# Kernel tuning notes

Hardware: AMD Instinct MI355X
Metric: run time of the kernel (lower is better)

## Reference

```python
import jax, jax.numpy as jnp
import numpy as np

D_MODEL = 1024
N_HEADS = 16
D_K = D_MODEL // N_HEADS


def setup_inputs() -> dict:
    key = jax.random.key(0)
    ks = jax.random.split(key, 7)
    B, T = 4, 2048
    scale = 1.0 / np.sqrt(D_MODEL)
    x = jax.random.normal(ks[0], (B, T, D_MODEL), dtype=jnp.float32)
    Wq = jax.random.uniform(ks[1], (D_MODEL, D_MODEL), jnp.float32, -scale, scale)
    Wk = jax.random.uniform(ks[2], (D_MODEL, D_MODEL), jnp.float32, -scale, scale)
    Wv = jax.random.uniform(ks[3], (D_MODEL, D_MODEL), jnp.float32, -scale, scale)
    bq = jax.random.uniform(ks[4], (D_MODEL,), jnp.float32, -scale, scale)
    bk = jax.random.uniform(ks[5], (D_MODEL,), jnp.float32, -scale, scale)
    bv = jax.random.uniform(ks[6], (D_MODEL,), jnp.float32, -scale, scale)
    return {"x": x, "Wq": Wq, "bq": bq, "Wk": Wk, "bk": bk, "Wv": Wv, "bv": bv}


def reference(x, Wq, bq, Wk, bk, Wv, bv):
    B, T, _ = x.shape
    # QKV projections -> (B, H, T, d_k)
    def split_heads(y):
        return y.reshape(B, T, N_HEADS, D_K).transpose(0, 2, 1, 3)
    Q = split_heads(x @ Wq + bq)
    K = split_heads(x @ Wk + bk)
    V = split_heads(x @ Wv + bv)
    scores = jnp.einsum('bhqd,bhkd->bhqk', Q, K) / jnp.sqrt(jnp.float32(D_K))
    # additive causal mask: -inf above the diagonal
    causal = jnp.tril(jnp.ones((T, T), dtype=bool))
    scores = jnp.where(causal, scores, -jnp.inf)
    attn = jax.nn.softmax(scores, axis=-1)
    out = jnp.einsum('bhqk,bhkd->bhqd', attn, V)
    return out.transpose(0, 2, 1, 3).reshape(B, T, D_MODEL)
```

## Files before the change

### kernel.cpp

```cpp
#include <hip/hip_runtime.h>
#include <hip/hip_bf16.h>

#define DM 1024
#define NH 16
#define DK 64
#define TT 2048
#define NBATCH 4
#define BT 8192

typedef __attribute__((ext_vector_type(8))) short short8;
typedef __attribute__((ext_vector_type(4))) float f32x4;
typedef unsigned short u16;

#define MFMA(a,b,c) __builtin_amdgcn_mfma_f32_16x16x32_bf16((a),(b),(c),0,0,0)

#define QSCALE 0.18033688011112684f

#define EXP2(x) __builtin_amdgcn_exp2f(x)

__device__ __forceinline__ u16 f2bf(float f){
  union { float f; unsigned u; } v; v.f = f;
  return (u16)((v.u + 0x7fffu + ((v.u >> 16) & 1u)) >> 16);
}

__device__ __forceinline__ unsigned cvtpk(float lo, float hi){
  unsigned r;
  asm("v_cvt_pk_bf16_f32 %0, %1, %2" : "=v"(r) : "v"(lo), "v"(hi));
  return r;
}

__device__ __forceinline__ void gload16(const void* g, void* l){
  __builtin_amdgcn_global_load_lds((__attribute__((address_space(1))) void*)(g),
                                   (__attribute__((address_space(3))) void*)(l), 16, 0, 0);
}

__device__ __forceinline__ float plmax(float x){
#if __has_builtin(__builtin_amdgcn_permlane16_swap) && __has_builtin(__builtin_amdgcn_permlane32_swap)
  auto r = __builtin_amdgcn_permlane16_swap(__float_as_uint(x), __float_as_uint(x), false, false);
  x = fmaxf(__uint_as_float(r[0]), __uint_as_float(r[1]));
  auto r2 = __builtin_amdgcn_permlane32_swap(__float_as_uint(x), __float_as_uint(x), false, false);
  x = fmaxf(__uint_as_float(r2[0]), __uint_as_float(r2[1]));
#else
  x = fmaxf(x, __shfl_xor(x, 16, 64));
  x = fmaxf(x, __shfl_xor(x, 32, 64));
#endif
  return x;
}

__device__ __forceinline__ float plsum(float x){
#if __has_builtin(__builtin_amdgcn_permlane16_swap) && __has_builtin(__builtin_amdgcn_permlane32_swap)
  auto r = __builtin_amdgcn_permlane16_swap(__float_as_uint(x), __float_as_uint(x), false, false);
  x = __uint_as_float(r[0]) + __uint_as_float(r[1]);
  auto r2 = __builtin_amdgcn_permlane32_swap(__float_as_uint(x), __float_as_uint(x), false, false);
  x = __uint_as_float(r2[0]) + __uint_as_float(r2[1]);
#else
  x = x + __shfl_xor(x, 16, 64);
  x = x + __shfl_xor(x, 32, 64);
#endif
  return x;
}

__global__ __launch_bounds__(256) void cvt_x(const float* __restrict__ x, u16* __restrict__ xb){
  int i = (blockIdx.x * 256 + threadIdx.x) * 4;
  float4 v = *(const float4*)(x + i);
  u16 o0 = f2bf(v.x), o1 = f2bf(v.y), o2 = f2bf(v.z), o3 = f2bf(v.w);
  ushort4 o; o.x=o0; o.y=o1; o.z=o2; o.w=o3;
  *(ushort4*)(xb + i) = o;
}

__global__ __launch_bounds__(256) void twp(
    const float* __restrict__ Wq, const float* __restrict__ Wk, const float* __restrict__ Wv,
    u16* __restrict__ wtq, u16* __restrict__ wtk, u16* __restrict__ wtv){
  const float* W = (blockIdx.z == 0) ? Wq : (blockIdx.z == 1) ? Wk : Wv;
  u16* wt = (blockIdx.z == 0) ? wtq : (blockIdx.z == 1) ? wtk : wtv;
  __shared__ float tile[32][33];
  int k0 = blockIdx.x * 32, n0 = blockIdx.y * 32;
  int tx = threadIdx.x & 31, ty = threadIdx.x >> 5;
  #pragma unroll
  for(int r = ty; r < 32; r += 8)
    tile[r][tx] = W[(size_t)(k0 + r) * DM + n0 + tx];
  __syncthreads();
  #pragma unroll
  for(int r = ty; r < 32; r += 8)
    wt[(size_t)(n0 + r) * DM + k0 + tx] = f2bf(tile[tx][r]);
}

__global__ __launch_bounds__(256) void qkv_gemm(
    const u16* __restrict__ xb,
    const u16* __restrict__ wtq, const u16* __restrict__ wtk, const u16* __restrict__ wtv,
    const float* __restrict__ bq, const float* __restrict__ bk, const float* __restrict__ bv,
    u16* __restrict__ qws, u16* __restrict__ kws, u16* __restrict__ vtws){
  __shared__ u16 sa[2][128 * 64];
  __shared__ u16 sb[2][128 * 64];
  const int id = blockIdx.x;
  const int idx = id >> 3;
  const int mt = (id & 7) * 8 + (idx & 7);
  const int y  = idx >> 3;
  const int m0 = mt * 128;
  const int ng = y * 128;
  const int mat = ng >> 10;
  const int n0 = ng & 1023;
  const u16* wt = (mat == 0) ? wtq : (mat == 1) ? wtk : wtv;
  const float* bias = (mat == 0) ? bq : (mat == 1) ? bk : bv;
  const int tid = threadIdx.x;
  const int lane = tid & 63, w = tid >> 6;
  const int wm = (w >> 1) * 64, wn = (w & 1) * 64;
  const int wbase0 = tid & 192;

  f32x4 acc[4][4] = {};

  #pragma unroll
  for(int p = 0; p < 4; p++){
    int base = p * 256 + wbase0;
    int idx2 = base + lane;
    int row = idx2 >> 3;
    int chs = (idx2 & 7) ^ (row & 7);
    gload16(xb + (size_t)(m0 + row) * 1024 + chs * 8, (char*)sa[0] + base * 16);
    gload16(wt + (size_t)(n0 + row) * 1024 + chs * 8, (char*)sb[0] + base * 16);
  }

  #pragma unroll 1
  for(int kt = 0; kt < 16; kt++){
    const int cur = kt & 1;
    __syncthreads();

    if(kt + 1 < 16){
      const int k0n = (kt + 1) * 64;
      #pragma unroll
      for(int p = 0; p < 4; p++){
        int base = p * 256 + wbase0;
        int idx2 = base + lane;
        int row = idx2 >> 3;
        int chs = (idx2 & 7) ^ (row & 7);
        gload16(xb + (size_t)(m0 + row) * 1024 + k0n + chs * 8, (char*)sa[cur ^ 1] + base * 16);
        gload16(wt + (size_t)(n0 + row) * 1024 + k0n + chs * 8, (char*)sb[cur ^ 1] + base * 16);
      }
    }

    #pragma unroll
    for(int ks = 0; ks < 2; ks++){
      short8 af[4], bfr[4];
      #pragma unroll
      for(int i = 0; i < 4; i++){
        int ra = wm + i * 16 + (lane & 15);
        int ca = ks * 64 + (lane >> 4) * 16;
        af[i] = *(const short8*)((const char*)sa[cur] + ra * 128 + (ca ^ ((ra & 7) << 4)));
        int rb = wn + i * 16 + (lane & 15);
        bfr[i] = *(const short8*)((const char*)sb[cur] + rb * 128 + (ca ^ ((rb & 7) << 4)));
      }
      __builtin_amdgcn_s_setprio(1);
      #pragma unroll
      for(int i = 0; i < 4; i++)
        #pragma unroll
        for(int j = 0; j < 4; j++)
          acc[i][j] = MFMA(af[i], bfr[j], acc[i][j]);
      __builtin_amdgcn_s_setprio(0);
    }
  }

  const float scl = (mat == 0) ? QSCALE : 1.0f;
  #pragma unroll
  for(int j = 0; j < 4; j++){
    int n = n0 + wn + j * 16 + (lane & 15);
    float bv_ = bias[n];
    int h = n >> 6, d = n & 63;
    #pragma unroll
    for(int i = 0; i < 4; i++){
      int mb = m0 + wm + i * 16 + (lane >> 4) * 4;
      int b = mb >> 11, t = mb & 2047;
      int bh = b * NH + h;
      if(mat == 2){
        ushort4 o4;
        o4.x = f2bf(acc[i][j][0] + bv_);
        o4.y = f2bf(acc[i][j][1] + bv_);
        o4.z = f2bf(acc[i][j][2] + bv_);
        o4.w = f2bf(acc[i][j][3] + bv_);
        int tp = (t & ~31) | (((t >> 2) & 3) << 3) | (((t >> 4) & 1) << 2);
        *(ushort4*)(vtws + ((size_t)bh * DK + d) * TT + tp) = o4;
      } else {
        u16* dst = (mat == 0) ? qws : kws;
        #pragma unroll
        for(int r = 0; r < 4; r++){
          u16 o = f2bf((acc[i][j][r] + bv_) * scl);
          dst[((size_t)bh * TT + t + r) * DK + d] = o;
        }
      }
    }
  }
}

__global__ __launch_bounds__(512) void attn(
    const u16* __restrict__ qws, const u16* __restrict__ kws, const u16* __restrict__ vtws,
    float* __restrict__ out){
  __shared__ u16 kt[2][64 * 64];
  __shared__ u16 vt[2][64 * 64];

  const int id = blockIdx.x;
  const int swz = (id & 7) * 64 + (id >> 3);
  const int qx = swz & 7;
  const int bh = swz >> 3;

  const int tid = threadIdx.x, lane = tid & 63, w = tid >> 6;
  const int g = lane >> 4, ln = lane & 15;
  const int b = bh >> 4, h = bh & 15;
  const u16* kbase = kws + (size_t)bh * TT * DK;
  const u16* vbase = vtws + (size_t)bh * DK * TT;
  const int sbase = tid & 448;
  const int srow = tid >> 3;
  const int schs = (tid & 7) ^ (srow & 7);

  #pragma unroll 1
  for(int qi = 0; qi < 2; qi++){
    const int qt = qi ? (15 - qx) : qx;
    const int q = qt * 128 + w * 16 + ln;

    short8 qf[2];
    {
      const u16* gq = qws + ((size_t)bh * TT + q) * DK + g * 8;
      qf[0] = *(const short8*)gq;
      qf[1] = *(const short8*)(gq + 32);
    }

    f32x4 o[4] = {};
    float m = -INFINITY, l = 0.f;

    const int nkt = 2 * qt + 2;
    const int myNkt = nkt - (w < 4 ? 1 : 0);

    __syncthreads();
    gload16(kbase + (size_t)srow * DK + schs * 8, (char*)kt[0] + sbase * 16);
    gload16(vbase + (size_t)srow * TT + schs * 8, (char*)vt[0] + sbase * 16);

    #pragma unroll 1
    for(int kti = 0; kti < nkt; kti++){
      const int cur = kti & 1;
      __syncthreads();

      if(kti + 1 < nkt){
        const int k0n = (kti + 1) * 64;
        gload16(kbase + (size_t)(k0n + srow) * DK + schs * 8, (char*)kt[cur ^ 1] + sbase * 16);
        gload16(vbase + (size_t)srow * TT + k0n + schs * 8, (char*)vt[cur ^ 1] + sbase * 16);
      }

      if(kti < myNkt){
        f32x4 s[4];
        __builtin_amdgcn_s_setprio(1);
        #pragma unroll
        for(int i = 0; i < 4; i++){
          f32x4 c = {};
          #pragma unroll
          for(int ks = 0; ks < 2; ks++){
            int rb = i * 16 + ln;
            int cb = ks * 64 + g * 16;
            short8 kfr = *(const short8*)((const char*)kt[cur] + rb * 128 + (cb ^ ((rb & 7) << 4)));
            c = MFMA(kfr, qf[ks], c);
          }
          s[i] = c;
        }
        __builtin_amdgcn_s_setprio(0);

        if(kti == myNkt - 1){
          const int k0 = kti * 64;
          #pragma unroll
          for(int i = 0; i < 4; i++)
            #pragma unroll
            for(int r = 0; r < 4; r++)
              if(k0 + i * 16 + g * 4 + r > q) s[i][r] = -INFINITY;
        }

        float mx0 = fmaxf(fmaxf(s[0][0], s[0][1]), fmaxf(s[0][2], s[0][3]));
        float mx1 = fmaxf(fmaxf(s[1][0], s[1][1]), fmaxf(s[1][2], s[1][3]));
        float mx2 = fmaxf(fmaxf(s[2][0], s[2][1]), fmaxf(s[2][2], s[2][3]));
        float mx3 = fmaxf(fmaxf(s[3][0], s[3][1]), fmaxf(s[3][2], s[3][3]));
        float pmax = fmaxf(fmaxf(mx0, mx1), fmaxf(mx2, mx3));
        pmax = plmax(pmax);

        if(!__all(pmax <= m + 8.f)){
          float mnew = fmaxf(m, pmax);
          float alpha = EXP2(m - mnew);
          l *= alpha;
          #pragma unroll
          for(int i = 0; i < 4; i++)
            #pragma unroll
            for(int r = 0; r < 4; r++) o[i][r] *= alpha;
          m = mnew;
        }

        #pragma unroll
        for(int i = 0; i < 4; i++)
          #pragma unroll
          for(int r = 0; r < 4; r++){
            float p = EXP2(s[i][r] - m);
            s[i][r] = p; l += p;
          }

        union PU { short8 s8; unsigned w[4]; };
        PU pb[2];
        #pragma unroll
        for(int ks = 0; ks < 2; ks++){
          pb[ks].w[0] = cvtpk(s[2*ks][0],   s[2*ks][1]);
          pb[ks].w[1] = cvtpk(s[2*ks][2],   s[2*ks][3]);
          pb[ks].w[2] = cvtpk(s[2*ks+1][0], s[2*ks+1][1]);
          pb[ks].w[3] = cvtpk(s[2*ks+1][2], s[2*ks+1][3]);
        }

        __builtin_amdgcn_s_setprio(1);
        #pragma unroll
        for(int i = 0; i < 4; i++){
          int dr = i * 16 + ln;
          const char* vrow = (const char*)vt[cur] + dr * 128;
          int sw = (dr & 7) << 4;
          #pragma unroll
          for(int ks = 0; ks < 2; ks++){
            short8 av = *(const short8*)(vrow + ((64 * ks + g * 16) ^ sw));
            o[i] = MFMA(av, pb[ks].s8, o[i]);
          }
        }
        __builtin_amdgcn_s_setprio(0);
      }
    }

    l = plsum(l);
    float inv = 1.0f / l;
    float* orow = out + ((size_t)(b * TT + q)) * DM + h * 64 + g * 4;
    #pragma unroll
    for(int i = 0; i < 4; i++){
      float4 v4;
      v4.x = o[i][0] * inv; v4.y = o[i][1] * inv;
      v4.z = o[i][2] * inv; v4.w = o[i][3] * inv;
      *(float4*)(orow + i * 16) = v4;
    }
  }
}

extern "C" void kernel_launch(void* const* d_in, const int* in_sizes, int n_in,
                              void* d_out, int out_size, void* d_ws, size_t ws_size,
                              hipStream_t stream){
  const float* x  = (const float*)d_in[0];
  const float* Wq = (const float*)d_in[1];
  const float* bq = (const float*)d_in[2];
  const float* Wk = (const float*)d_in[3];
  const float* bk = (const float*)d_in[4];
  const float* Wv = (const float*)d_in[5];
  const float* bv = (const float*)d_in[6];
  float* out = (float*)d_out;

  char* ws = (char*)d_ws;
  u16* xb   = (u16*)(ws);
  u16* wtq  = (u16*)(ws + (16u << 20));
  u16* wtk  = (u16*)(ws + (18u << 20));
  u16* wtv  = (u16*)(ws + (20u << 20));
  u16* qws  = (u16*)(ws + (22u << 20));
  u16* kws  = (u16*)(ws + (38u << 20));
  u16* vtws = (u16*)(ws + (54u << 20));

  cvt_x<<<dim3(BT * DM / 1024), dim3(256), 0, stream>>>(x, xb);
  twp<<<dim3(32, 32, 3), dim3(256), 0, stream>>>(Wq, Wk, Wv, wtq, wtk, wtv);
  qkv_gemm<<<dim3(1536), dim3(256), 0, stream>>>(xb, wtq, wtk, wtv, bq, bk, bv, qws, kws, vtws);
  attn<<<dim3(512), dim3(512), 0, stream>>>(qws, kws, vtws, out);
}
```

Measured before the change: 143.6 us.

## Switch attention to 32x32x16 MFMA with 32 queries per wave

Rewrites the attention inner loop to use 32x32x16 bf16 MFMA tiles, so each wave handles 32 query rows and the block shrinks from 8 to 4 waves. The P matrix is repacked across half-waves with permlane32 swaps, and the V layout permutation in the projection epilogue is removed to match. The aim is to cut LDS reads and cross-lane reductions per FLOP and raise MFMA efficiency. In exchange it uses more accumulator registers per wave and may lower occupancy and latency hiding.

```diff
diff --git a/kernel.cpp b/kernel.cpp
--- a/kernel.cpp
+++ b/kernel.cpp
@@ -10,13 +10,17 @@
 
 typedef __attribute__((ext_vector_type(8))) short short8;
 typedef __attribute__((ext_vector_type(4))) float f32x4;
+typedef __attribute__((ext_vector_type(16))) float f32x16;
 typedef unsigned short u16;
 
-#define MFMA(a,b,c) __builtin_amdgcn_mfma_f32_16x16x32_bf16((a),(b),(c),0,0,0)
+#define MFMA(a,b,c)   __builtin_amdgcn_mfma_f32_16x16x32_bf16((a),(b),(c),0,0,0)
+#define MFMA32(a,b,c) __builtin_amdgcn_mfma_f32_32x32x16_bf16((a),(b),(c),0,0,0)
 
 #define QSCALE 0.18033688011112684f
 
 #define EXP2(x) __builtin_amdgcn_exp2f(x)
+
+#define HAS_PLSWAP (__has_builtin(__builtin_amdgcn_permlane32_swap))
 
 __device__ __forceinline__ u16 f2bf(float f){
   union { float f; unsigned u; } v; v.f = f;
@@ -34,30 +38,33 @@
                                    (__attribute__((address_space(3))) void*)(l), 16, 0, 0);
 }
 
-__device__ __forceinline__ float plmax(float x){
-#if __has_builtin(__builtin_amdgcn_permlane16_swap) && __has_builtin(__builtin_amdgcn_permlane32_swap)
-  auto r = __builtin_amdgcn_permlane16_swap(__float_as_uint(x), __float_as_uint(x), false, false);
-  x = fmaxf(__uint_as_float(r[0]), __uint_as_float(r[1]));
-  auto r2 = __builtin_amdgcn_permlane32_swap(__float_as_uint(x), __float_as_uint(x), false, false);
-  x = fmaxf(__uint_as_float(r2[0]), __uint_as_float(r2[1]));
+__device__ __forceinline__ float plmax32(float x){
+#if HAS_PLSWAP
+  auto r = __builtin_amdgcn_permlane32_swap(__float_as_uint(x), __float_as_uint(x), false, false);
+  return fmaxf(__uint_as_float(r[0]), __uint_as_float(r[1]));
 #else
-  x = fmaxf(x, __shfl_xor(x, 16, 64));
-  x = fmaxf(x, __shfl_xor(x, 32, 64));
+  return fmaxf(x, __shfl_xor(x, 32, 64));
 #endif
-  return x;
-}
-
-__device__ __forceinline__ float plsum(float x){
-#if __has_builtin(__builtin_amdgcn_permlane16_swap) && __has_builtin(__builtin_amdgcn_permlane32_swap)
-  auto r = __builtin_amdgcn_permlane16_swap(__float_as_uint(x), __float_as_uint(x), false, false);
-  x = __uint_as_float(r[0]) + __uint_as_float(r[1]);
-  auto r2 = __builtin_amdgcn_permlane32_swap(__float_as_uint(x), __float_as_uint(x), false, false);
-  x = __uint_as_float(r2[0]) + __uint_as_float(r2[1]);
+}
+__device__ __forceinline__ float plsum32(float x){
+#if HAS_PLSWAP
+  auto r = __builtin_amdgcn_permlane32_swap(__float_as_uint(x), __float_as_uint(x), false, false);
+  return __uint_as_float(r[0]) + __uint_as_float(r[1]);
 #else
-  x = x + __shfl_xor(x, 16, 64);
-  x = x + __shfl_xor(x, 32, 64);
+  return x + __shfl_xor(x, 32, 64);
 #endif
-  return x;
+}
+
+__device__ __forceinline__ void plpack(unsigned A, unsigned C, unsigned& wlo, unsigned& whi){
+#if HAS_PLSWAP
+  auto r = __builtin_amdgcn_permlane32_swap(A, C, false, false);
+  wlo = r[0]; whi = r[1];
+#else
+  unsigned pa = __shfl_xor(A, 32, 64), pc = __shfl_xor(C, 32, 64);
+  int hi = (threadIdx.x & 32) != 0;
+  wlo = hi ? pc : A;
+  whi = hi ? C : pa;
+#endif
 }
 
 __global__ __launch_bounds__(256) void cvt_x(const float* __restrict__ x, u16* __restrict__ xb){
@@ -175,8 +182,7 @@
         o4.y = f2bf(acc[i][j][1] + bv_);
         o4.z = f2bf(acc[i][j][2] + bv_);
         o4.w = f2bf(acc[i][j][3] + bv_);
-        int tp = (t & ~31) | (((t >> 2) & 3) << 3) | (((t >> 4) & 1) << 2);
-        *(ushort4*)(vtws + ((size_t)bh * DK + d) * TT + tp) = o4;
+        *(ushort4*)(vtws + ((size_t)bh * DK + d) * TT + t) = o4;
       } else {
         u16* dst = (mat == 0) ? qws : kws;
         #pragma unroll
@@ -189,7 +195,7 @@
   }
 }
 
-__global__ __launch_bounds__(512) void attn(
+__global__ __launch_bounds__(256) void attn(
     const u16* __restrict__ qws, const u16* __restrict__ kws, const u16* __restrict__ vtws,
     float* __restrict__ out){
   __shared__ u16 kt[2][64 * 64];
@@ -201,35 +207,38 @@
   const int bh = swz >> 3;
 
   const int tid = threadIdx.x, lane = tid & 63, w = tid >> 6;
-  const int g = lane >> 4, ln = lane & 15;
+  const int hi = lane >> 5, lq = lane & 31;
   const int b = bh >> 4, h = bh & 15;
   const u16* kbase = kws + (size_t)bh * TT * DK;
   const u16* vbase = vtws + (size_t)bh * DK * TT;
-  const int sbase = tid & 448;
-  const int srow = tid >> 3;
-  const int schs = (tid & 7) ^ (srow & 7);
+  const int sw0 = (lq & 7) << 4;
 
   #pragma unroll 1
   for(int qi = 0; qi < 2; qi++){
     const int qt = qi ? (15 - qx) : qx;
-    const int q = qt * 128 + w * 16 + ln;
-
-    short8 qf[2];
+    const int q = qt * 128 + w * 32 + lq;
+
+    short8 qf[4];
     {
-      const u16* gq = qws + ((size_t)bh * TT + q) * DK + g * 8;
-      qf[0] = *(const short8*)gq;
-      qf[1] = *(const short8*)(gq + 32);
-    }
-
-    f32x4 o[4] = {};
+      const u16* gq = qws + ((size_t)bh * TT + q) * DK + hi * 8;
+      #pragma unroll
+      for(int s = 0; s < 4; s++) qf[s] = *(const short8*)(gq + s * 16);
+    }
+
+    f32x16 o0 = {}, o1 = {};
     float m = -INFINITY, l = 0.f;
 
     const int nkt = 2 * qt + 2;
-    const int myNkt = nkt - (w < 4 ? 1 : 0);
+    const int myNkt = 2 * qt + (w >> 1) + 1;
 
     __syncthreads();
-    gload16(kbase + (size_t)srow * DK + schs * 8, (char*)kt[0] + sbase * 16);
-    gload16(vbase + (size_t)srow * TT + schs * 8, (char*)vt[0] + sbase * 16);
+    #pragma unroll
+    for(int p = 0; p < 2; p++){
+      int base = p * 256 + (tid & 192);
+      int ci = base + lane, row = ci >> 3, chs = (ci & 7) ^ (row & 7);
+      gload16(kbase + (size_t)row * DK + chs * 8, (char*)kt[0] + base * 16);
+      gload16(vbase + (size_t)row * TT + chs * 8, (char*)vt[0] + base * 16);
+    }
 
     #pragma unroll 1
     for(int kti = 0; kti < nkt; kti++){
@@ -238,97 +247,114 @@
 
       if(kti + 1 < nkt){
         const int k0n = (kti + 1) * 64;
-        gload16(kbase + (size_t)(k0n + srow) * DK + schs * 8, (char*)kt[cur ^ 1] + sbase * 16);
-        gload16(vbase + (size_t)srow * TT + k0n + schs * 8, (char*)vt[cur ^ 1] + sbase * 16);
+        #pragma unroll
+        for(int p = 0; p < 2; p++){
+          int base = p * 256 + (tid & 192);
+          int ci = base + lane, row = ci >> 3, chs = (ci & 7) ^ (row & 7);
+          gload16(kbase + (size_t)(k0n + row) * DK + chs * 8, (char*)kt[cur ^ 1] + base * 16);
+          gload16(vbase + (size_t)row * TT + k0n + chs * 8, (char*)vt[cur ^ 1] + base * 16);
+        }
       }
 
       if(kti < myNkt){
-        f32x4 s[4];
+        f32x16 s0 = {}, s1 = {};
         __builtin_amdgcn_s_setprio(1);
         #pragma unroll
-        for(int i = 0; i < 4; i++){
-          f32x4 c = {};
-          #pragma unroll
-          for(int ks = 0; ks < 2; ks++){
-            int rb = i * 16 + ln;
-            int cb = ks * 64 + g * 16;
-            short8 kfr = *(const short8*)((const char*)kt[cur] + rb * 128 + (cb ^ ((rb & 7) << 4)));
-            c = MFMA(kfr, qf[ks], c);
-          }
-          s[i] = c;
+        for(int s = 0; s < 4; s++){
+          int colb = 32 * s + 16 * hi;
+          short8 k0f = *(const short8*)((const char*)kt[cur] + lq * 128 + (colb ^ sw0));
+          short8 k1f = *(const short8*)((const char*)kt[cur] + (32 + lq) * 128 + (colb ^ sw0));
+          s0 = MFMA32(k0f, qf[s], s0);
+          s1 = MFMA32(k1f, qf[s], s1);
         }
         __builtin_amdgcn_s_setprio(0);
 
         if(kti == myNkt - 1){
           const int k0 = kti * 64;
           #pragma unroll
-          for(int i = 0; i < 4; i++)
-            #pragma unroll
-            for(int r = 0; r < 4; r++)
-              if(k0 + i * 16 + g * 4 + r > q) s[i][r] = -INFINITY;
-        }
-
-        float mx0 = fmaxf(fmaxf(s[0][0], s[0][1]), fmaxf(s[0][2], s[0][3]));
-        float mx1 = fmaxf(fmaxf(s[1][0], s[1][1]), fmaxf(s[1][2], s[1][3]));
-        float mx2 = fmaxf(fmaxf(s[2][0], s[2][1]), fmaxf(s[2][2], s[2][3]));
-        float mx3 = fmaxf(fmaxf(s[3][0], s[3][1]), fmaxf(s[3][2], s[3][3]));
-        float pmax = fmaxf(fmaxf(mx0, mx1), fmaxf(mx2, mx3));
-        pmax = plmax(pmax);
+          for(int r = 0; r < 16; r++){
+            int key = k0 + (r & 3) + 8 * (r >> 2) + 4 * hi;
+            if(key > q)      s0[r] = -INFINITY;
+            if(key + 32 > q) s1[r] = -INFINITY;
+          }
+        }
+
+        float px0, px1, px2, px3, px4, px5, px6, px7;
+        px0 = fmaxf(fmaxf(s0[0], s0[1]),  fmaxf(s0[2], s0[3]));
+        px1 = fmaxf(fmaxf(s0[4], s0[5]),  fmaxf(s0[6], s0[7]));
+        px2 = fmaxf(fmaxf(s0[8], s0[9]),  fmaxf(s0[10], s0[11]));
+        px3 = fmaxf(fmaxf(s0[12], s0[13]), fmaxf(s0[14], s0[15]));
+        px4 = fmaxf(fmaxf(s1[0], s1[1]),  fmaxf(s1[2], s1[3]));
+        px5 = fmaxf(fmaxf(s1[4], s1[5]),  fmaxf(s1[6], s1[7]));
+        px6 = fmaxf(fmaxf(s1[8], s1[9]),  fmaxf(s1[10], s1[11]));
+        px7 = fmaxf(fmaxf(s1[12], s1[13]), fmaxf(s1[14], s1[15]));
+        float pmax = fmaxf(fmaxf(fmaxf(px0, px1), fmaxf(px2, px3)),
+                           fmaxf(fmaxf(px4, px5), fmaxf(px6, px7)));
+        pmax = plmax32(pmax);
 
         if(!__all(pmax <= m + 8.f)){
           float mnew = fmaxf(m, pmax);
           float alpha = EXP2(m - mnew);
           l *= alpha;
           #pragma unroll
-          for(int i = 0; i < 4; i++)
-            #pragma unroll
-            for(int r = 0; r < 4; r++) o[i][r] *= alpha;
+          for(int r = 0; r < 16; r++){ o0[r] *= alpha; o1[r] *= alpha; }
           m = mnew;
         }
 
         #pragma unroll
-        for(int i = 0; i < 4; i++)
-          #pragma unroll
-          for(int r = 0; r < 4; r++){
-            float p = EXP2(s[i][r] - m);
-            s[i][r] = p; l += p;
+        for(int r = 0; r < 16; r++){
+          float p0 = EXP2(s0[r] - m); s0[r] = p0;
+          float p1 = EXP2(s1[r] - m); s1[r] = p1;
+          l += p0 + p1;
+        }
+
+        union PU { short8 s8; unsigned u[4]; };
+        PU pb[4];
+        #pragma unroll
+        for(int s = 0; s < 4; s++){
+          const int u_ = s & 1;
+          unsigned A, B, C2, D2;
+          if((s >> 1) == 0){
+            A  = cvtpk(s0[8*u_ + 0], s0[8*u_ + 1]);
+            B  = cvtpk(s0[8*u_ + 2], s0[8*u_ + 3]);
+            C2 = cvtpk(s0[8*u_ + 4], s0[8*u_ + 5]);
+            D2 = cvtpk(s0[8*u_ + 6], s0[8*u_ + 7]);
+          } else {
+            A  = cvtpk(s1[8*u_ + 0], s1[8*u_ + 1]);
+            B  = cvtpk(s1[8*u_ + 2], s1[8*u_ + 3]);
+            C2 = cvtpk(s1[8*u_ + 4], s1[8*u_ + 5]);
+            D2 = cvtpk(s1[8*u_ + 6], s1[8*u_ + 7]);
           }
-
-        union PU { short8 s8; unsigned w[4]; };
-        PU pb[2];
-        #pragma unroll
-        for(int ks = 0; ks < 2; ks++){
-          pb[ks].w[0] = cvtpk(s[2*ks][0],   s[2*ks][1]);
-          pb[ks].w[1] = cvtpk(s[2*ks][2],   s[2*ks][3]);
-          pb[ks].w[2] = cvtpk(s[2*ks+1][0], s[2*ks+1][1]);
-          pb[ks].w[3] = cvtpk(s[2*ks+1][2], s[2*ks+1][3]);
+          plpack(A, C2, pb[s].u[0], pb[s].u[2]);
+          plpack(B, D2, pb[s].u[1], pb[s].u[3]);
         }
 
         __builtin_amdgcn_s_setprio(1);
         #pragma unroll
-        for(int i = 0; i < 4; i++){
-          int dr = i * 16 + ln;
-          const char* vrow = (const char*)vt[cur] + dr * 128;
-          int sw = (dr & 7) << 4;
-          #pragma unroll
-          for(int ks = 0; ks < 2; ks++){
-            short8 av = *(const short8*)(vrow + ((64 * ks + g * 16) ^ sw));
-            o[i] = MFMA(av, pb[ks].s8, o[i]);
-          }
+        for(int s = 0; s < 4; s++){
+          int colb = 32 * s + 16 * hi;
+          short8 v0 = *(const short8*)((const char*)vt[cur] + lq * 128 + (colb ^ sw0));
+          short8 v1 = *(const short8*)((const char*)vt[cur] + (32 + lq) * 128 + (colb ^ sw0));
+          o0 = MFMA32(v0, pb[s].s8, o0);
+          o1 = MFMA32(v1, pb[s].s8, o1);
         }
         __builtin_amdgcn_s_setprio(0);
       }
     }
 
-    l = plsum(l);
+    l = plsum32(l);
     float inv = 1.0f / l;
-    float* orow = out + ((size_t)(b * TT + q)) * DM + h * 64 + g * 4;
+    float* orow = out + ((size_t)(b * TT + q)) * DM + h * 64;
     #pragma unroll
-    for(int i = 0; i < 4; i++){
+    for(int rq = 0; rq < 4; rq++){
       float4 v4;
-      v4.x = o[i][0] * inv; v4.y = o[i][1] * inv;
-      v4.z = o[i][2] * inv; v4.w = o[i][3] * inv;
-      *(float4*)(orow + i * 16) = v4;
+      v4.x = o0[4*rq + 0] * inv; v4.y = o0[4*rq + 1] * inv;
+      v4.z = o0[4*rq + 2] * inv; v4.w = o0[4*rq + 3] * inv;
+      *(float4*)(orow + rq * 8 + hi * 4) = v4;
+      float4 v5;
+      v5.x = o1[4*rq + 0] * inv; v5.y = o1[4*rq + 1] * inv;
+      v5.z = o1[4*rq + 2] * inv; v5.w = o1[4*rq + 3] * inv;
+      *(float4*)(orow + 32 + rq * 8 + hi * 4) = v5;
     }
   }
 }
@@ -357,5 +383,5 @@
   cvt_x<<<dim3(BT * DM / 1024), dim3(256), 0, stream>>>(x, xb);
   twp<<<dim3(32, 32, 3), dim3(256), 0, stream>>>(Wq, Wk, Wv, wtq, wtk, wtv);
   qkv_gemm<<<dim3(1536), dim3(256), 0, stream>>>(xb, wtq, wtk, wtv, bq, bk, bv, qws, kws, vtws);
-  attn<<<dim3(512), dim3(512), 0, stream>>>(qws, kws, vtws, out);
-}
+  attn<<<dim3(512), dim3(256), 0, stream>>>(qws, kws, vtws, out);
+}
```

Result: slower. 153.3 us (+6.7%).

## Process two query sub-tiles per wave in attention, dropping paired q-tile scheduling

Applied to the files above, without the earlier changes.

The attention kernel moves from 512-thread blocks that each handle two complementary q-tiles in sequence to 256-thread blocks that each handle one 128-row q-tile, with every wave carrying two 16-row query groups (A and B). Each K/V fragment read from LDS now feeds two MFMA streams, which halves LDS reads per unit of compute and raises instruction-level parallelism. Blocks are ordered longest-first by q-tile and grouped by XCD. In exchange, each wave holds roughly twice the accumulator registers, and the causal load balancing now relies on block scheduling order instead of pairing.

```diff
diff --git a/kernel.cpp b/kernel.cpp
--- a/kernel.cpp
+++ b/kernel.cpp
@@ -189,147 +189,199 @@
   }
 }
 
-__global__ __launch_bounds__(512) void attn(
+__global__ __launch_bounds__(256) void attn(
     const u16* __restrict__ qws, const u16* __restrict__ kws, const u16* __restrict__ vtws,
     float* __restrict__ out){
   __shared__ u16 kt[2][64 * 64];
   __shared__ u16 vt[2][64 * 64];
 
   const int id = blockIdx.x;
-  const int swz = (id & 7) * 64 + (id >> 3);
-  const int qx = swz & 7;
-  const int bh = swz >> 3;
+  const int xcd = id & 7, local = id >> 3;
+  const int qt = 15 - (local >> 3);
+  const int bh = xcd * 8 + (local & 7);
 
   const int tid = threadIdx.x, lane = tid & 63, w = tid >> 6;
   const int g = lane >> 4, ln = lane & 15;
   const int b = bh >> 4, h = bh & 15;
   const u16* kbase = kws + (size_t)bh * TT * DK;
   const u16* vbase = vtws + (size_t)bh * DK * TT;
-  const int sbase = tid & 448;
-  const int srow = tid >> 3;
-  const int schs = (tid & 7) ^ (srow & 7);
+
+  const int qA = qt * 128 + w * 16 + ln;
+  const int qB = qA + 64;
+
+  short8 qfA[2], qfB[2];
+  {
+    const u16* gq = qws + ((size_t)bh * TT + qA) * DK + g * 8;
+    qfA[0] = *(const short8*)gq;
+    qfA[1] = *(const short8*)(gq + 32);
+    const u16* gq2 = qws + ((size_t)bh * TT + qB) * DK + g * 8;
+    qfB[0] = *(const short8*)gq2;
+    qfB[1] = *(const short8*)(gq2 + 32);
+  }
+
+  f32x4 oA[4] = {}, oB[4] = {};
+  float mA = -INFINITY, lA = 0.f;
+  float mB = -INFINITY, lB = 0.f;
+
+  const int nkt = 2 * qt + 2;
+
+  #pragma unroll
+  for(int p = 0; p < 2; p++){
+    int base = p * 256 + (tid & 192);
+    int ci = base + lane, row = ci >> 3, chs = (ci & 7) ^ (row & 7);
+    gload16(kbase + (size_t)row * DK + chs * 8, (char*)kt[0] + base * 16);
+    gload16(vbase + (size_t)row * TT + chs * 8, (char*)vt[0] + base * 16);
+  }
 
   #pragma unroll 1
-  for(int qi = 0; qi < 2; qi++){
-    const int qt = qi ? (15 - qx) : qx;
-    const int q = qt * 128 + w * 16 + ln;
-
-    short8 qf[2];
-    {
-      const u16* gq = qws + ((size_t)bh * TT + q) * DK + g * 8;
-      qf[0] = *(const short8*)gq;
-      qf[1] = *(const short8*)(gq + 32);
-    }
-
-    f32x4 o[4] = {};
-    float m = -INFINITY, l = 0.f;
-
-    const int nkt = 2 * qt + 2;
-    const int myNkt = nkt - (w < 4 ? 1 : 0);
-
+  for(int kti = 0; kti < nkt; kti++){
+    const int cur = kti & 1;
     __syncthreads();
-    gload16(kbase + (size_t)srow * DK + schs * 8, (char*)kt[0] + sbase * 16);
-    gload16(vbase + (size_t)srow * TT + schs * 8, (char*)vt[0] + sbase * 16);
-
-    #pragma unroll 1
-    for(int kti = 0; kti < nkt; kti++){
-      const int cur = kti & 1;
-      __syncthreads();
-
-      if(kti + 1 < nkt){
-        const int k0n = (kti + 1) * 64;
-        gload16(kbase + (size_t)(k0n + srow) * DK + schs * 8, (char*)kt[cur ^ 1] + sbase * 16);
-        gload16(vbase + (size_t)srow * TT + k0n + schs * 8, (char*)vt[cur ^ 1] + sbase * 16);
-      }
-
-      if(kti < myNkt){
-        f32x4 s[4];
-        __builtin_amdgcn_s_setprio(1);
-        #pragma unroll
-        for(int i = 0; i < 4; i++){
-          f32x4 c = {};
-          #pragma unroll
-          for(int ks = 0; ks < 2; ks++){
-            int rb = i * 16 + ln;
-            int cb = ks * 64 + g * 16;
-            short8 kfr = *(const short8*)((const char*)kt[cur] + rb * 128 + (cb ^ ((rb & 7) << 4)));
-            c = MFMA(kfr, qf[ks], c);
-          }
-          s[i] = c;
-        }
-        __builtin_amdgcn_s_setprio(0);
-
-        if(kti == myNkt - 1){
-          const int k0 = kti * 64;
-          #pragma unroll
-          for(int i = 0; i < 4; i++)
-            #pragma unroll
-            for(int r = 0; r < 4; r++)
-              if(k0 + i * 16 + g * 4 + r > q) s[i][r] = -INFINITY;
-        }
-
-        float mx0 = fmaxf(fmaxf(s[0][0], s[0][1]), fmaxf(s[0][2], s[0][3]));
-        float mx1 = fmaxf(fmaxf(s[1][0], s[1][1]), fmaxf(s[1][2], s[1][3]));
-        float mx2 = fmaxf(fmaxf(s[2][0], s[2][1]), fmaxf(s[2][2], s[2][3]));
-        float mx3 = fmaxf(fmaxf(s[3][0], s[3][1]), fmaxf(s[3][2], s[3][3]));
-        float pmax = fmaxf(fmaxf(mx0, mx1), fmaxf(mx2, mx3));
-        pmax = plmax(pmax);
-
-        if(!__all(pmax <= m + 8.f)){
-          float mnew = fmaxf(m, pmax);
-          float alpha = EXP2(m - mnew);
-          l *= alpha;
-          #pragma unroll
-          for(int i = 0; i < 4; i++)
-            #pragma unroll
-            for(int r = 0; r < 4; r++) o[i][r] *= alpha;
-          m = mnew;
-        }
-
+
+    if(kti + 1 < nkt){
+      const int k0n = (kti + 1) * 64;
+      #pragma unroll
+      for(int p = 0; p < 2; p++){
+        int base = p * 256 + (tid & 192);
+        int ci = base + lane, row = ci >> 3, chs = (ci & 7) ^ (row & 7);
+        gload16(kbase + (size_t)(k0n + row) * DK + chs * 8, (char*)kt[cur ^ 1] + base * 16);
+        gload16(vbase + (size_t)row * TT + k0n + chs * 8, (char*)vt[cur ^ 1] + base * 16);
+      }
+    }
+
+    const bool doA = (kti < nkt - 1);
+
+    f32x4 sA[4], sB[4];
+    __builtin_amdgcn_s_setprio(1);
+    #pragma unroll
+    for(int i = 0; i < 4; i++){
+      f32x4 cA = {}, cB = {};
+      #pragma unroll
+      for(int ks = 0; ks < 2; ks++){
+        int rb = i * 16 + ln;
+        int cb = ks * 64 + g * 16;
+        short8 kfr = *(const short8*)((const char*)kt[cur] + rb * 128 + (cb ^ ((rb & 7) << 4)));
+        if(doA) cA = MFMA(kfr, qfA[ks], cA);
+        cB = MFMA(kfr, qfB[ks], cB);
+      }
+      sA[i] = cA; sB[i] = cB;
+    }
+    __builtin_amdgcn_s_setprio(0);
+
+    const int k0 = kti * 64;
+    if(doA && kti == nkt - 2){
+      #pragma unroll
+      for(int i = 0; i < 4; i++)
+        #pragma unroll
+        for(int r = 0; r < 4; r++)
+          if(k0 + i * 16 + g * 4 + r > qA) sA[i][r] = -INFINITY;
+    }
+    if(kti == nkt - 1){
+      #pragma unroll
+      for(int i = 0; i < 4; i++)
+        #pragma unroll
+        for(int r = 0; r < 4; r++)
+          if(k0 + i * 16 + g * 4 + r > qB) sB[i][r] = -INFINITY;
+    }
+
+    union PU { short8 s8; unsigned u[4]; };
+    PU pbA[2], pbB[2];
+
+    if(doA){
+      float mx0 = fmaxf(fmaxf(sA[0][0], sA[0][1]), fmaxf(sA[0][2], sA[0][3]));
+      float mx1 = fmaxf(fmaxf(sA[1][0], sA[1][1]), fmaxf(sA[1][2], sA[1][3]));
+      float mx2 = fmaxf(fmaxf(sA[2][0], sA[2][1]), fmaxf(sA[2][2], sA[2][3]));
+      float mx3 = fmaxf(fmaxf(sA[3][0], sA[3][1]), fmaxf(sA[3][2], sA[3][3]));
+      float pmax = plmax(fmaxf(fmaxf(mx0, mx1), fmaxf(mx2, mx3)));
+      if(!__all(pmax <= mA + 8.f)){
+        float mnew = fmaxf(mA, pmax);
+        float alpha = EXP2(mA - mnew);
+        lA *= alpha;
         #pragma unroll
         for(int i = 0; i < 4; i++)
           #pragma unroll
-          for(int r = 0; r < 4; r++){
-            float p = EXP2(s[i][r] - m);
-            s[i][r] = p; l += p;
-          }
-
-        union PU { short8 s8; unsigned w[4]; };
-        PU pb[2];
-        #pragma unroll
-        for(int ks = 0; ks < 2; ks++){
-          pb[ks].w[0] = cvtpk(s[2*ks][0],   s[2*ks][1]);
-          pb[ks].w[1] = cvtpk(s[2*ks][2],   s[2*ks][3]);
-          pb[ks].w[2] = cvtpk(s[2*ks+1][0], s[2*ks+1][1]);
-          pb[ks].w[3] = cvtpk(s[2*ks+1][2], s[2*ks+1][3]);
+          for(int r = 0; r < 4; r++) oA[i][r] *= alpha;
+        mA = mnew;
+      }
+      #pragma unroll
+      for(int i = 0; i < 4; i++)
+        #pragma unroll
+        for(int r = 0; r < 4; r++){
+          float p = EXP2(sA[i][r] - mA);
+          sA[i][r] = p; lA += p;
         }
-
-        __builtin_amdgcn_s_setprio(1);
-        #pragma unroll
-        for(int i = 0; i < 4; i++){
-          int dr = i * 16 + ln;
-          const char* vrow = (const char*)vt[cur] + dr * 128;
-          int sw = (dr & 7) << 4;
+      #pragma unroll
+      for(int ks = 0; ks < 2; ks++){
+        pbA[ks].u[0] = cvtpk(sA[2*ks][0],   sA[2*ks][1]);
+        pbA[ks].u[1] = cvtpk(sA[2*ks][2],   sA[2*ks][3]);
+        pbA[ks].u[2] = cvtpk(sA[2*ks+1][0], sA[2*ks+1][1]);
+        pbA[ks].u[3] = cvtpk(sA[2*ks+1][2], sA[2*ks+1][3]);
+      }
+    }
+
+    {
+      float mx0 = fmaxf(fmaxf(sB[0][0], sB[0][1]), fmaxf(sB[0][2], sB[0][3]));
+      float mx1 = fmaxf(fmaxf(sB[1][0], sB[1][1]), fmaxf(sB[1][2], sB[1][3]));
+      float mx2 = fmaxf(fmaxf(sB[2][0], sB[2][1]), fmaxf(sB[2][2], sB[2][3]));
+      float mx3 = fmaxf(fmaxf(sB[3][0], sB[3][1]), fmaxf(sB[3][2], sB[3][3]));
+      float pmax = plmax(fmaxf(fmaxf(mx0, mx1), fmaxf(mx2, mx3)));
+      if(!__all(pmax <= mB + 8.f)){
+        float mnew = fmaxf(mB, pmax);
+        float alpha = EXP2(mB - mnew);
+        lB *= alpha;
+        #pragma unroll
+        for(int i = 0; i < 4; i++)
           #pragma unroll
-          for(int ks = 0; ks < 2; ks++){
-            short8 av = *(const short8*)(vrow + ((64 * ks + g * 16) ^ sw));
-            o[i] = MFMA(av, pb[ks].s8, o[i]);
-          }
+          for(int r = 0; r < 4; r++) oB[i][r] *= alpha;
+        mB = mnew;
+      }
+      #pragma unroll
+      for(int i = 0; i < 4; i++)
+        #pragma unroll
+        for(int r = 0; r < 4; r++){
+          float p = EXP2(sB[i][r] - mB);
+          sB[i][r] = p; lB += p;
         }
-        __builtin_amdgcn_s_setprio(0);
-      }
-    }
-
-    l = plsum(l);
-    float inv = 1.0f / l;
-    float* orow = out + ((size_t)(b * TT + q)) * DM + h * 64 + g * 4;
+      #pragma unroll
+      for(int ks = 0; ks < 2; ks++){
+        pbB[ks].u[0] = cvtpk(sB[2*ks][0],   sB[2*ks][1]);
+        pbB[ks].u[1] = cvtpk(sB[2*ks][2],   sB[2*ks][3]);
+        pbB[ks].u[2] = cvtpk(sB[2*ks+1][0], sB[2*ks+1][1]);
+        pbB[ks].u[3] = cvtpk(sB[2*ks+1][2], sB[2*ks+1][3]);
+      }
+    }
+
+    __builtin_amdgcn_s_setprio(1);
     #pragma unroll
     for(int i = 0; i < 4; i++){
-      float4 v4;
-      v4.x = o[i][0] * inv; v4.y = o[i][1] * inv;
-      v4.z = o[i][2] * inv; v4.w = o[i][3] * inv;
-      *(float4*)(orow + i * 16) = v4;
-    }
+      int dr = i * 16 + ln;
+      const char* vrow = (const char*)vt[cur] + dr * 128;
+      int sw = (dr & 7) << 4;
+      #pragma unroll
+      for(int ks = 0; ks < 2; ks++){
+        short8 av = *(const short8*)(vrow + ((64 * ks + g * 16) ^ sw));
+        if(doA) oA[i] = MFMA(av, pbA[ks].s8, oA[i]);
+        oB[i] = MFMA(av, pbB[ks].s8, oB[i]);
+      }
+    }
+    __builtin_amdgcn_s_setprio(0);
+  }
+
+  lA = plsum(lA);
+  lB = plsum(lB);
+  float invA = 1.0f / lA, invB = 1.0f / lB;
+  float* orowA = out + ((size_t)(b * TT + qA)) * DM + h * 64 + g * 4;
+  float* orowB = out + ((size_t)(b * TT + qB)) * DM + h * 64 + g * 4;
+  #pragma unroll
+  for(int i = 0; i < 4; i++){
+    float4 v4;
+    v4.x = oA[i][0] * invA; v4.y = oA[i][1] * invA;
+    v4.z = oA[i][2] * invA; v4.w = oA[i][3] * invA;
+    *(float4*)(orowA + i * 16) = v4;
+    float4 v5;
+    v5.x = oB[i][0] * invB; v5.y = oB[i][1] * invB;
+    v5.z = oB[i][2] * invB; v5.w = oB[i][3] * invB;
+    *(float4*)(orowB + i * 16) = v5;
   }
 }
 
@@ -357,5 +409,5 @@
   cvt_x<<<dim3(BT * DM / 1024), dim3(256), 0, stream>>>(x, xb);
   twp<<<dim3(32, 32, 3), dim3(256), 0, stream>>>(Wq, Wk, Wv, wtq, wtk, wtv);
   qkv_gemm<<<dim3(1536), dim3(256), 0, stream>>>(xb, wtq, wtk, wtv, bq, bk, bv, qws, kws, vtws);
-  attn<<<dim3(512), dim3(512), 0, stream>>>(qws, kws, vtws, out);
-}
+  attn<<<dim3(1024), dim3(256), 0, stream>>>(qws, kws, vtws, out);
+}
```

Measured after the change: 161.2 us. +12.2%, slower.
